# Kernel optimization log

Measured on AMD Instinct MI355X. Metric: run time of the kernel, lower is better.

The kernel has to match this reference:

```python
import jax, jax.numpy as jnp
import numpy as np

B, N, IN_DIM, HID, K = 16, 1024, 512, 256, 3
ALPHA = 0.2  # leaky relu slope
NEG = -9e15  # mask value from original code (-9000000000000000.0)


def setup_inputs() -> dict:
    key = jax.random.key(0)
    ks = jax.random.split(key, 10)
    adj = (jax.random.uniform(ks[0], (B, 3, N, N)) < 0.01).astype(jnp.float32)
    inputs = jax.random.normal(ks[1], (B, N, IN_DIM), dtype=jnp.float32)
    s = 0.07
    W = jax.random.normal(ks[2], (3, K, IN_DIM, HID), dtype=jnp.float32) * s
    # attention vector a [2F,1] split into a1 (for h_i) and a2 (for h_j)
    a1 = jax.random.normal(ks[3], (3, K, HID), dtype=jnp.float32) * s
    a2 = jax.random.normal(ks[4], (3, K, HID), dtype=jnp.float32) * s
    Ww = jax.random.normal(ks[5], (HID, 100), dtype=jnp.float32) * s
    bw = jnp.zeros((100,), dtype=jnp.float32)
    Wc = jax.random.normal(ks[6], (100, 1), dtype=jnp.float32) * s
    return {"adj": adj, "inputs": inputs, "W": W, "a1": a1, "a2": a2,
            "Ww": Ww, "bw": bw, "Wc": Wc}


def _gat(adjp, inputs, W_, a1_, a2_):
    # h = X W : [B,N,F]
    h = jnp.einsum('bni,if->bnf', inputs, W_)
    # e_ij = leakyrelu(a1.h_i + a2.h_j) -- equivalent to the original
    # cat([h_i, h_j]) @ a without materializing the [B,N,N,2F] tensor
    f1 = h @ a1_  # [B,N]
    f2 = h @ a2_  # [B,N]
    e = jax.nn.leaky_relu(f1[:, :, None] + f2[:, None, :], ALPHA)
    att = jax.nn.softmax(jnp.where(adjp > 0, e, NEG), axis=2)
    # (dropout on attention is identity in eval mode)
    return jnp.einsum('bnm,bmf->bnf', att, h)


def reference(adj, inputs, W, a1, a2, Ww, bw, Wc):
    k_layers = W.shape[1]
    # powers[t] holds adj_t^(k+1) for layer k (matmuls(adj, k))
    powers = [adj[:, t] for t in range(3)]
    layer_list = []
    for k in range(k_layers):
        out = 0.0
        for t in range(3):
            out = out + _gat(powers[t], inputs, W[t, k], a1[t, k], a2[t, k])
        layer_list.append(out)
        if k + 1 < k_layers:
            powers = [jnp.matmul(p, adj[:, t]) for t, p in enumerate(powers)]
    H = jnp.stack(layer_list, axis=2)  # [B,N,K,F]
    s = jnp.tanh(H @ Ww + bw) @ Wc     # [B,N,K,1]
    vs = jax.nn.softmax(s[..., 0], axis=2)  # [B,N,K]
    return jnp.einsum('bnk,bnkf->bnf', vs, H)
```

## Files before the change

### kernel.cpp

```cpp
#include <hip/hip_runtime.h>


typedef unsigned long long u64;
typedef __attribute__((ext_vector_type(4))) float f32x4;
typedef __attribute__((ext_vector_type(8))) short bf16x8;

#define NEGF (-9.0e15f)
#define L2E 1.44269504f

__device__ __forceinline__ float fexp2(float x){
#if __has_builtin(__builtin_amdgcn_exp2f)
  return __builtin_amdgcn_exp2f(x);
#else
  return exp2f(x);
#endif
}
__device__ __forceinline__ float frcp(float x){
#if __has_builtin(__builtin_amdgcn_rcpf)
  return __builtin_amdgcn_rcpf(x);
#else
  return 1.0f/x;
#endif
}
__device__ __forceinline__ unsigned short f2bf(float x){
  union { float f; unsigned u; } a; a.f = x;
  unsigned r = a.u + 0x7FFFu + ((a.u >> 16) & 1u);
  return (unsigned short)(r >> 16);
}
__device__ __forceinline__ unsigned pack_bf16x2(float lo, float hi){
  union { float f; unsigned u; } a, b; a.f = lo; b.f = hi;
  unsigned ul = a.u + 0x8000u, uh = b.u + 0x8000u;
#if __has_builtin(__builtin_amdgcn_perm)
  return __builtin_amdgcn_perm(uh, ul, 0x07060302u);
#else
  return (ul >> 16) | (uh & 0xFFFF0000u);
#endif
}
__device__ __forceinline__ float tanh_fast(float x){
  float e = fexp2(x * 2.885390082f);
  return 1.0f - 2.0f*frcp(e + 1.0f);
}
__device__ __forceinline__ void async_cp16(void* lds, const void* g){
  __builtin_amdgcn_global_load_lds(
      (const __attribute__((address_space(1))) unsigned int*)g,
      (__attribute__((address_space(3))) unsigned int*)lds, 16, 0, 0);
}


__global__ void k_build_wb(const float* __restrict__ W, const float* __restrict__ a1,
                           const float* __restrict__ a2, unsigned short* __restrict__ Wb)
{
  int idx = blockIdx.x*256 + threadIdx.x;
  if (idx >= 64*2432) return;
  int c = idx % 2432, g = idx / 2432;
  unsigned short o[8];
  if (c < 2304) {
    int s = c >> 8, f = c & 255, t = s % 3, klq = s / 3;
    const float* wp = W + ((size_t)(t*3 + klq)*512)*256 + f;
#pragma unroll
    for (int e = 0; e < 8; ++e) o[e] = f2bf(wp[(size_t)(g*8 + e)*256]);
  } else if (c < 2322) {
    int c2 = c - 2304, s = c2 >> 1, t = s % 3, klq = s / 3;
    const float* av = ((c2 & 1) ? a2 : a1) + (t*3 + klq)*256;
    const float* wp = W + ((size_t)(t*3 + klq)*512)*256;
#pragma unroll
    for (int e = 0; e < 8; ++e) {
      float acc = 0.0f;
      const float* wr = wp + (size_t)(g*8 + e)*256;
      for (int f = 0; f < 256; ++f) acc += wr[f]*av[f];
      o[e] = f2bf(acc);
    }
  } else {
#pragma unroll
    for (int e = 0; e < 8; ++e) o[e] = 0;
  }
  ushort4 lo, hi;
  lo.x=o[0]; lo.y=o[1]; lo.z=o[2]; lo.w=o[3];
  hi.x=o[4]; hi.y=o[5]; hi.z=o[6]; hi.w=o[7];
  ushort4* dst = (ushort4*)(Wb + (size_t)idx*8);
  dst[0] = lo; dst[1] = hi;
}

__global__ void k_xconv(const float* __restrict__ X, unsigned short* __restrict__ Xs)
{
  int idx = blockIdx.x*256 + threadIdx.x;
  int bn = idx & 16383, g = idx >> 14;
  const float* xp = X + (size_t)bn*512 + g*8;
  ushort4 lo, hi;
  lo.x=f2bf(xp[0]); lo.y=f2bf(xp[1]); lo.z=f2bf(xp[2]); lo.w=f2bf(xp[3]);
  hi.x=f2bf(xp[4]); hi.y=f2bf(xp[5]); hi.z=f2bf(xp[6]); hi.w=f2bf(xp[7]);
  ushort4* dst = (ushort4*)(Xs + (size_t)idx*8);
  dst[0] = lo; dst[1] = hi;
}

__global__ __launch_bounds__(256) void k_bitpack(
    const float* __restrict__ adj, u64* __restrict__ mbA0, u64* __restrict__ mbT)
{
  int gw = blockIdx.x*4 + (threadIdx.x >> 6);
  int lane = threadIdx.x & 63;
#pragma unroll
  for (int r = 0; r < 2; ++r) {
    int row = gw*2 + r;
    int i = row & 1023, bt = row >> 10;
    int t = bt % 3, b = bt / 3;
    int sb = t*16 + b;
    const float* ap = adj + (size_t)row*1024 + lane;
    u64 myw = 0;
#pragma unroll
    for (int w = 0; w < 16; ++w) {
      u64 bal = __ballot(ap[w*64] > 0.0f);
      if (lane == w) myw = bal;
    }
    if (lane < 16) {
      mbA0[((size_t)sb*1024 + i)*16 + lane] = myw;
      mbT[((size_t)sb*16 + lane)*1024 + i] = myw;
    }
  }
}

__global__ void k_boolmm(const u64* __restrict__ A, const u64* __restrict__ Bm,
                         u64* __restrict__ outA, u64* __restrict__ outT, int sbase)
{
  int tid = blockIdx.x*256 + threadIdx.x;
  int w = tid & 15, i = (tid >> 4) & 1023, tb = tid >> 14;
  const u64* Ar = A + ((size_t)tb*1024 + i)*16;
  const u64* Bb = Bm + (size_t)tb*16384;
  u64 acc = 0;
  for (int ww = 0; ww < 16; ++ww) {
    u64 aw = Ar[ww];
    while (aw) {
      int kk = __builtin_ctzll(aw);
      aw &= aw - 1;
      acc |= Bb[((size_t)(ww*64 + kk))*16 + w];
    }
  }
  if (outA) outA[((size_t)tb*1024 + i)*16 + w] = acc;
  int t = tb >> 4, bq = tb & 15;
  outT[(((size_t)(sbase + t)*16 + bq)*16 + w)*1024 + i] = acc;
}


__global__ __launch_bounds__(256) void k_gemm_h(
    const unsigned short* __restrict__ Xs, const unsigned short* __restrict__ Wb,
    unsigned short* __restrict__ hsw, float* __restrict__ fbuf,
    float* __restrict__ G1p, float* __restrict__ G2p)
{
  __shared__ unsigned short Asl[8*132*8 + 8];
  __shared__ unsigned short Bsl[8*132*8 + 8];
  const int tid = threadIdx.x, lane = tid & 63, wid = tid >> 6;
  int vb = blockIdx.x;
  int xc = vb & 7, mrest = vb >> 3;
  int mt = xc + 8*(mrest/19), nt = mrest % 19;
  const int M0 = mt << 7, N0 = nt << 7;
  const int wr = (wid >> 1) << 6, wc = (wid & 1) << 6;
  const int me = lane & 15;
  f32x4 acc[4][4] = {};
  for (int ks64 = 0; ks64 < 8; ++ks64) {
    __syncthreads();
#pragma unroll
    for (int c = 0; c < 4; ++c) {
      int chunk = wid*4 + c, g = chunk >> 1, hh = chunk & 1;
      int ldsoff = (g*132 + hh*64)*8;
      const unsigned short* gpA = Xs + ((size_t)(ks64*8 + g)*16384 + (M0 + hh*64 + lane))*8;
      async_cp16(Asl + ldsoff, gpA);
      const unsigned short* gpB = Wb + ((size_t)(ks64*8 + g)*2432 + (N0 + hh*64 + lane))*8;
      async_cp16(Bsl + ldsoff, gpB);
    }
    __syncthreads();
#pragma unroll
    for (int ks32 = 0; ks32 < 2; ++ks32) {
      const int kg = ks32*4 + (lane >> 4);
      bf16x8 afr[4], bfr[4];
#pragma unroll
      for (int rb = 0; rb < 4; ++rb)
        afr[rb] = *(const bf16x8*)(Asl + (kg*132 + wr + rb*16 + me)*8);
#pragma unroll
      for (int cb = 0; cb < 4; ++cb)
        bfr[cb] = *(const bf16x8*)(Bsl + (kg*132 + wc + cb*16 + me)*8);
#pragma unroll
      for (int rb = 0; rb < 4; ++rb)
#pragma unroll
        for (int cb = 0; cb < 4; ++cb)
          acc[rb][cb] = __builtin_amdgcn_mfma_f32_16x16x32_bf16(afr[rb], bfr[cb], acc[rb][cb], 0, 0, 0);
    }
  }
  const int quad = lane >> 4;
#pragma unroll
  for (int rb = 0; rb < 4; ++rb) {
    int jbase = M0 + wr + rb*16 + quad*4;
    int bidx = jbase >> 10, jn = jbase & 1023;
#pragma unroll
    for (int cb = 0; cb < 4; ++cb) {
      int c = N0 + wc + cb*16 + me;
      f32x4 v = acc[rb][cb];
      if (c < 2304) {
        int s = c >> 8, f = c & 255;
        ushort4 pk;
        pk.x = f2bf(v[0]); pk.y = f2bf(v[1]); pk.z = f2bf(v[2]); pk.w = f2bf(v[3]);
        *(ushort4*)(hsw + (size_t)s*4194304 + (size_t)bidx*262144 + ((jn>>3)*256 + f)*8 + (jn&7)) = pk;
      } else if (c < 2322) {
        int c2 = c - 2304, s = c2 >> 1, wh = c2 & 1;
        f32x4 vL = v * L2E;
        if (wh == 0) {
          *(f32x4*)(fbuf + (size_t)s*16384 + jbase) = vL;
        } else {
          f32x4 g1v, g2v;
#pragma unroll
          for (int k = 0; k < 4; ++k) {
            g1v[k] = fexp2(vL[k]);
            g2v[k] = fexp2(0.2f*vL[k]);
          }
          *(f32x4*)(G1p + (size_t)s*16384 + jbase) = g1v;
          *(f32x4*)(G2p + (size_t)s*16384 + jbase) = g2v;
        }
      }
    }
  }
}


__global__ __launch_bounds__(256) void k_rowl(
    const u64* __restrict__ mbT, const float* __restrict__ fbuf,
    const float* __restrict__ G1p, const float* __restrict__ G2p,
    float* __restrict__ rowR1, float* __restrict__ rowR2,
    float* __restrict__ rowRT, float* __restrict__ rowZr)
{
  int lane = threadIdx.x & 63;
  for (int gw = blockIdx.x*4 + (threadIdx.x >> 6); gw < 147456; gw += 18432) {
    int i = gw & 1023, sb = gw >> 10;
    int b = sb & 15, s = sb >> 4;

    const float* g1q = G1p + (size_t)s*16384 + b*1024 + lane*16;
    const float* g2q = G2p + (size_t)s*16384 + b*1024 + lane*16;
    float4 a0 = *(const float4*)(g1q);
    float4 a1 = *(const float4*)(g1q + 4);
    float4 a2 = *(const float4*)(g1q + 8);
    float4 a3 = *(const float4*)(g1q + 12);
    float4 c0 = *(const float4*)(g2q);
    float4 c1 = *(const float4*)(g2q + 4);
    float4 c2 = *(const float4*)(g2q + 8);
    float4 c3 = *(const float4*)(g2q + 12);
    float g1e[16] = {a0.x,a0.y,a0.z,a0.w, a1.x,a1.y,a1.z,a1.w,
                     a2.x,a2.y,a2.z,a2.w, a3.x,a3.y,a3.z,a3.w};
    float g2e[16] = {c0.x,c0.y,c0.z,c0.w, c1.x,c1.y,c1.z,c1.w,
                     c2.x,c2.y,c2.z,c2.w, c3.x,c3.y,c3.z,c3.w};

    u64 word = mbT[(size_t)sb*16384 + (size_t)(lane >> 2)*1024 + i];
    unsigned fld = (unsigned)(word >> ((lane & 3)*16)) & 0xFFFFu;

    float f1i = fbuf[(size_t)s*16384 + b*1024 + i];
    float RT = fexp2(-f1i);

    float S1 = 0.0f, S2 = 0.0f;
#pragma unroll
    for (int e = 0; e < 16; ++e) {
      unsigned m32 = (unsigned)(((int)(fld << (31 - e))) >> 31);
      float t1 = __uint_as_float(__float_as_uint(g1e[e]) & m32);
      float t2 = __uint_as_float(__float_as_uint(g2e[e]) & m32);
      bool c = (g1e[e] >= RT);
      S1 += c ? t1 : 0.0f;
      S2 += c ? 0.0f : t2;
    }
#pragma unroll
    for (int off = 32; off; off >>= 1) {
      S1 += __shfl_xor(S1, off);
      S2 += __shfl_xor(S2, off);
    }
    if (lane == 0) {
      float EF1 = fexp2(f1i);
      float EF2 = fexp2(0.2f*f1i);
      float l = __builtin_fmaf(EF1, S1, EF2*S2);
      float rinv = frcp(l);
      rowR1[gw] = EF1*rinv;
      rowR2[gw] = EF2*rinv;
      rowRT[gw] = RT;
      rowZr[gw] = (l == 0.0f) ? 0.0009765625f : 0.0f;
    }
  }
}


__global__ __launch_bounds__(256, 3) void k_attgemm(
    const unsigned short* __restrict__ hsw,
    const float* __restrict__ G1p, const float* __restrict__ G2p,
    const float* __restrict__ rowR1, const float* __restrict__ rowR2,
    const float* __restrict__ rowRT, const float* __restrict__ rowZr,
    const u64* __restrict__ mbT, float* __restrict__ H32)
{
  __shared__ unsigned short Bts[2*8192];
  const int tid = threadIdx.x, lane = tid & 63, wid = tid >> 6;
  const int me = lane & 15, quad = lane >> 4;
  int vb = blockIdx.x;
  int mt = vb / 48, g = vb % 48;
  int kl = g >> 4, b = g & 15;
  const int i0w = mt*64 + wid*16;
  const int ir0 = i0w + me;
  const unsigned short* hbase = hsw + (size_t)(kl*3)*4194304 + (size_t)b*262144;
  const float* g1b = G1p + (size_t)(kl*3)*16384 + b*1024;
  const float* g2b = G2p + (size_t)(kl*3)*16384 + b*1024;
  const float* R1b = rowR1 + ((kl*3)*16 + b)*1024;
  const float* R2b = rowR2 + ((kl*3)*16 + b)*1024;
  const float* RTb = rowRT + ((kl*3)*16 + b)*1024;
  const float* Zrb = rowZr + ((kl*3)*16 + b)*1024;
  const u64* mb = mbT + (size_t)((kl*3)*16 + b)*16384;

  float R1v, R2v, RTv;
  unsigned Zru;
  f32x4 acc[16] = {};

  {
    const unsigned short* hstage = hbase + wid*2048;
    unsigned short* lb = Bts + wid*2048;
#pragma unroll
    for (int c = 0; c < 4; ++c)
      async_cp16(lb + c*512, hstage + c*512 + lane*8);
  }
  u64 mw = mb[ir0];
  u64 nm = 0;

  for (int it = 0; it < 96; ++it) {
    const int tt = it >> 5, kk = it & 1;
    const int st = (it >> 1) & 15;
    if ((it & 31) == 0) {
      R1v = R1b[tt*16384 + ir0];
      R2v = R2b[tt*16384 + ir0];
      RTv = RTb[tt*16384 + ir0];
      Zru = __float_as_uint(Zrb[tt*16384 + ir0]);
    }
    if (!kk && it) mw = nm;

    __syncthreads();

    if (it + 1 < 96) {
      int nx = it + 1;
      int nt2 = nx >> 5, ns = (nx >> 1) & 15, nk = nx & 1;
      const unsigned short* hstage = hbase + (size_t)nt2*4194304 + ns*16384 + (nk*4 + wid)*2048;
      unsigned short* lb = Bts + nk*8192 + wid*2048;
#pragma unroll
      for (int c = 0; c < 4; ++c)
        async_cp16(lb + c*512, hstage + c*512 + lane*8);
    }
    if (kk && it + 1 < 96) {
      int gid = (it + 1) >> 1;
      int nt2 = gid >> 4, ns = gid & 15;
      nm = mb[(size_t)nt2*262144 + ns*1024 + ir0];
    }

    const int joff = tt*16384 + st*64 + kk*32 + quad*8;
    float4 ga = *(const float4*)(g1b + joff);
    float4 gb4 = *(const float4*)(g1b + joff + 4);
    float4 ha = *(const float4*)(g2b + joff);
    float4 hb4 = *(const float4*)(g2b + joff + 4);
    float g1e[8] = {ga.x, ga.y, ga.z, ga.w, gb4.x, gb4.y, gb4.z, gb4.w};
    float g2e[8] = {ha.x, ha.y, ha.z, ha.w, hb4.x, hb4.y, hb4.z, hb4.w};

    const int kloc = kk*32 + quad*8;
    unsigned mby = (unsigned)((mw >> kloc) & 0xFFull);
    union { bf16x8 v; unsigned u[4]; } ua;
#pragma unroll
    for (int p = 0; p < 4; ++p) {
      float p0, p1;
      {
        const int e = 2*p;
        bool c = (g1e[e] >= RTv);
        float pu = (c ? g1e[e] : g2e[e]) * (c ? R1v : R2v);
        unsigned m32 = (unsigned)(((int)(mby << (31 - e))) >> 31);
        p0 = __uint_as_float((__float_as_uint(pu) & m32) | Zru);
      }
      {
        const int e = 2*p + 1;
        bool c = (g1e[e] >= RTv);
        float pu = (c ? g1e[e] : g2e[e]) * (c ? R1v : R2v);
        unsigned m32 = (unsigned)(((int)(mby << (31 - e))) >> 31);
        p1 = __uint_as_float((__float_as_uint(pu) & m32) | Zru);
      }
      ua.u[p] = pack_bf16x2(p0, p1);
    }
    const unsigned short* bbase = Bts + kk*8192 + quad*2048;
#pragma unroll
    for (int cb = 0; cb < 16; ++cb) {
      bf16x8 bf = *(const bf16x8*)(bbase + (cb*16 + me)*8);
      acc[cb] = __builtin_amdgcn_mfma_f32_16x16x32_bf16(ua.v, bf, acc[cb], 0, 0, 0);
    }
  }

  {
    int io = i0w + quad*4;
#pragma unroll
    for (int cb = 0; cb < 16; ++cb) {
      int f = cb*16 + me;
      float* hp = H32 + (((size_t)b*1024 + io)*3 + kl)*256 + f;
#pragma unroll
      for (int r = 0; r < 4; ++r)
        hp[(size_t)r*768] = acc[cb][r];
    }
  }
}


__global__ __launch_bounds__(256) void k_score(
    const float* __restrict__ H32, const float* __restrict__ Ww,
    const float* __restrict__ bwv, const float* __restrict__ Wcv, float* __restrict__ svals)
{
  __shared__ unsigned short Bs[8*7*64*8];
  __shared__ float bwL[128], WcL[128];
  const int tid = threadIdx.x, lane = tid & 63, wid = tid >> 6;
  const int me = lane & 15, quad = lane >> 4;
  for (int idx = tid; idx < 3584; idx += 256) {
    int kk = idx / 448, rem = idx % 448;
    int cb = rem >> 6, l = rem & 63;
    int n = cb*16 + (l & 15);
    int kbase = kk*32 + (l >> 4)*8;
    ushort4 lo, hi;
    if (n < 100) {
      const float* wp = Ww + (size_t)kbase*100 + n;
      lo.x = f2bf(wp[0]);   lo.y = f2bf(wp[100]); lo.z = f2bf(wp[200]); lo.w = f2bf(wp[300]);
      hi.x = f2bf(wp[400]); hi.y = f2bf(wp[500]); hi.z = f2bf(wp[600]); hi.w = f2bf(wp[700]);
    } else {
      lo.x=lo.y=lo.z=lo.w=0; hi.x=hi.y=hi.z=hi.w=0;
    }
    ushort4* dst = (ushort4*)(Bs + (size_t)idx*8);
    dst[0] = lo; dst[1] = hi;
  }
  if (tid < 128) {
    bwL[tid] = (tid < 100) ? bwv[tid] : 0.0f;
    WcL[tid] = (tid < 100) ? Wcv[tid] : 0.0f;
  }
  __syncthreads();

  const int row0 = blockIdx.x*64 + wid*16;
  const float* Arow = H32 + (size_t)(row0 + me)*256;
  f32x4 acc[7] = {};
#pragma unroll
  for (int kk = 0; kk < 8; ++kk) {
    const float* ap = Arow + kk*32 + quad*8;
    float4 a0 = *(const float4*)(ap);
    float4 a1 = *(const float4*)(ap + 4);
    union { bf16x8 v; unsigned u[4]; } ua;
    ua.u[0] = pack_bf16x2(a0.x, a0.y);
    ua.u[1] = pack_bf16x2(a0.z, a0.w);
    ua.u[2] = pack_bf16x2(a1.x, a1.y);
    ua.u[3] = pack_bf16x2(a1.z, a1.w);
#pragma unroll
    for (int cb = 0; cb < 7; ++cb) {
      bf16x8 bf = *(const bf16x8*)(Bs + ((size_t)(kk*7 + cb)*64 + lane)*8);
      acc[cb] = __builtin_amdgcn_mfma_f32_16x16x32_bf16(ua.v, bf, acc[cb], 0, 0, 0);
    }
  }
#pragma unroll
  for (int r = 0; r < 4; ++r) {
    float contrib = 0.0f;
#pragma unroll
    for (int cb = 0; cb < 7; ++cb) {
      int col = cb*16 + me;
      contrib += tanh_fast(acc[cb][r] + bwL[col]) * WcL[col];
    }
    contrib += __shfl_xor(contrib, 1);
    contrib += __shfl_xor(contrib, 2);
    contrib += __shfl_xor(contrib, 4);
    contrib += __shfl_xor(contrib, 8);
    if (me == 0) svals[row0 + quad*4 + r] = contrib;
  }
}

__global__ void k_combine(const float* __restrict__ svals, const float* __restrict__ H32,
                          float* __restrict__ out)
{
  int tid = blockIdx.x*256 + threadIdx.x;
  int fq = tid & 63, bn = tid >> 6;
  float s0 = svals[bn*3], s1 = svals[bn*3+1], s2 = svals[bn*3+2];
  float mm = fmaxf(s0, fmaxf(s1, s2));
  float e0 = fexp2((s0-mm)*L2E), e1 = fexp2((s1-mm)*L2E), e2 = fexp2((s2-mm)*L2E);
  float inv = frcp(e0 + e1 + e2);
  const f32x4* h0 = (const f32x4*)(H32 + (size_t)bn*768) + fq;
  const f32x4* h1 = (const f32x4*)(H32 + (size_t)bn*768 + 256) + fq;
  const f32x4* h2 = (const f32x4*)(H32 + (size_t)bn*768 + 512) + fq;
  f32x4 r = (e0*(*h0) + e1*(*h1) + e2*(*h2))*inv;
  *((f32x4*)out + (size_t)bn*64 + fq) = r;
}


extern "C" void kernel_launch(void* const* d_in, const int* in_sizes, int n_in,
                              void* d_out, int out_size, void* d_ws, size_t ws_size,
                              hipStream_t stream) {
  const float* adj = (const float*)d_in[0];
  const float* X   = (const float*)d_in[1];
  const float* W   = (const float*)d_in[2];
  const float* a1  = (const float*)d_in[3];
  const float* a2  = (const float*)d_in[4];
  const float* Ww  = (const float*)d_in[5];
  const float* bw  = (const float*)d_in[6];
  const float* Wc  = (const float*)d_in[7];
  float* out = (float*)d_out;
  char* ws = (char*)d_ws;

  unsigned short* Xs  = (unsigned short*)(ws + 0);
  unsigned short* Wb  = (unsigned short*)(ws + 16777216);
  float* H32          = (float*)(ws + 0);
  unsigned short* hsw = (unsigned short*)(ws + 50331648);
  u64* mbA            = (u64*)(ws + 125829120);
  float* rowR1        = (float*)(ws + 125829120);
  float* rowR2        = (float*)(ws + 126418944);
  float* rowRT        = (float*)(ws + 127008768);
  float* rowZr        = (float*)(ws + 127598592);
  u64* mbT            = (u64*)(ws + 138412032);
  float* fbuf         = (float*)(ws + 157286400);
  float* G1p          = (float*)(ws + 158466048);
  float* G2p          = (float*)(ws + 159055872);
  float* svals        = (float*)(ws + 159645696);

  k_build_wb<<<608, 256, 0, stream>>>(W, a1, a2, Wb);
  k_xconv<<<4096, 256, 0, stream>>>(X, Xs);
  k_bitpack<<<6144, 256, 0, stream>>>(adj, mbA, mbT);
  k_boolmm<<<3072, 256, 0, stream>>>(mbA, mbA, mbA + 786432, mbT, 3);
  k_boolmm<<<3072, 256, 0, stream>>>(mbA, mbA + 786432, (u64*)nullptr, mbT, 6);
  k_gemm_h<<<2432, 256, 0, stream>>>(Xs, Wb, hsw, fbuf, G1p, G2p);
  k_rowl<<<4608, 256, 0, stream>>>(mbT, fbuf, G1p, G2p, rowR1, rowR2, rowRT, rowZr);
  k_attgemm<<<768, 256, 0, stream>>>(hsw, G1p, G2p, rowR1, rowR2, rowRT, rowZr, mbT, H32);
  k_score<<<768, 256, 0, stream>>>(H32, Ww, bw, Wc, svals);
  k_combine<<<4096, 256, 0, stream>>>(svals, H32, out);
}
```

Before: 435.0 us.

## Merge prep kernels, overlap first boolean matmul with H GEMM, fuse score+combine

Three independent preprocessing kernels (weight pack, X conversion, adjacency bitpack) are merged into one launch with block-range dispatch. The first boolean adjacency-power kernel now runs as extra blocks of the H GEMM launch so the two can overlap. The score and combine kernels are fused, with 384-thread blocks covering 32 nodes and the scores kept in shared memory. This removes launch gaps and the svals round trip, at the cost of shared-memory allocation in the boolmm blocks and uneven block workloads.

```diff
diff --git a/kernel.cpp b/kernel.cpp
--- a/kernel.cpp
+++ b/kernel.cpp
@@ -47,76 +47,76 @@
 }
 
 
-__global__ void k_build_wb(const float* __restrict__ W, const float* __restrict__ a1,
-                           const float* __restrict__ a2, unsigned short* __restrict__ Wb)
-{
-  int idx = blockIdx.x*256 + threadIdx.x;
-  if (idx >= 64*2432) return;
-  int c = idx % 2432, g = idx / 2432;
-  unsigned short o[8];
-  if (c < 2304) {
-    int s = c >> 8, f = c & 255, t = s % 3, klq = s / 3;
-    const float* wp = W + ((size_t)(t*3 + klq)*512)*256 + f;
-#pragma unroll
-    for (int e = 0; e < 8; ++e) o[e] = f2bf(wp[(size_t)(g*8 + e)*256]);
-  } else if (c < 2322) {
-    int c2 = c - 2304, s = c2 >> 1, t = s % 3, klq = s / 3;
-    const float* av = ((c2 & 1) ? a2 : a1) + (t*3 + klq)*256;
-    const float* wp = W + ((size_t)(t*3 + klq)*512)*256;
-#pragma unroll
-    for (int e = 0; e < 8; ++e) {
-      float acc = 0.0f;
-      const float* wr = wp + (size_t)(g*8 + e)*256;
-      for (int f = 0; f < 256; ++f) acc += wr[f]*av[f];
-      o[e] = f2bf(acc);
-    }
-  } else {
-#pragma unroll
-    for (int e = 0; e < 8; ++e) o[e] = 0;
-  }
-  ushort4 lo, hi;
-  lo.x=o[0]; lo.y=o[1]; lo.z=o[2]; lo.w=o[3];
-  hi.x=o[4]; hi.y=o[5]; hi.z=o[6]; hi.w=o[7];
-  ushort4* dst = (ushort4*)(Wb + (size_t)idx*8);
-  dst[0] = lo; dst[1] = hi;
-}
-
-__global__ void k_xconv(const float* __restrict__ X, unsigned short* __restrict__ Xs)
-{
-  int idx = blockIdx.x*256 + threadIdx.x;
-  int bn = idx & 16383, g = idx >> 14;
-  const float* xp = X + (size_t)bn*512 + g*8;
-  ushort4 lo, hi;
-  lo.x=f2bf(xp[0]); lo.y=f2bf(xp[1]); lo.z=f2bf(xp[2]); lo.w=f2bf(xp[3]);
-  hi.x=f2bf(xp[4]); hi.y=f2bf(xp[5]); hi.z=f2bf(xp[6]); hi.w=f2bf(xp[7]);
-  ushort4* dst = (ushort4*)(Xs + (size_t)idx*8);
-  dst[0] = lo; dst[1] = hi;
-}
-
-__global__ __launch_bounds__(256) void k_bitpack(
+__global__ __launch_bounds__(256) void k_prep(
+    const float* __restrict__ W, const float* __restrict__ a1,
+    const float* __restrict__ a2, unsigned short* __restrict__ Wb,
+    const float* __restrict__ X, unsigned short* __restrict__ Xs,
     const float* __restrict__ adj, u64* __restrict__ mbA0, u64* __restrict__ mbT)
 {
-  int gw = blockIdx.x*4 + (threadIdx.x >> 6);
-  int lane = threadIdx.x & 63;
-#pragma unroll
-  for (int r = 0; r < 2; ++r) {
-    int row = gw*2 + r;
-    int i = row & 1023, bt = row >> 10;
-    int t = bt % 3, b = bt / 3;
-    int sb = t*16 + b;
-    const float* ap = adj + (size_t)row*1024 + lane;
-    u64 myw = 0;
-#pragma unroll
-    for (int w = 0; w < 16; ++w) {
-      u64 bal = __ballot(ap[w*64] > 0.0f);
-      if (lane == w) myw = bal;
-    }
-    if (lane < 16) {
-      mbA0[((size_t)sb*1024 + i)*16 + lane] = myw;
-      mbT[((size_t)sb*16 + lane)*1024 + i] = myw;
-    }
-  }
-}
+  if (blockIdx.x < 608) {
+    int idx = blockIdx.x*256 + threadIdx.x;
+    if (idx >= 64*2432) return;
+    int c = idx % 2432, g = idx / 2432;
+    unsigned short o[8];
+    if (c < 2304) {
+      int s = c >> 8, f = c & 255, t = s % 3, klq = s / 3;
+      const float* wp = W + ((size_t)(t*3 + klq)*512)*256 + f;
+#pragma unroll
+      for (int e = 0; e < 8; ++e) o[e] = f2bf(wp[(size_t)(g*8 + e)*256]);
+    } else if (c < 2322) {
+      int c2 = c - 2304, s = c2 >> 1, t = s % 3, klq = s / 3;
+      const float* av = ((c2 & 1) ? a2 : a1) + (t*3 + klq)*256;
+      const float* wp = W + ((size_t)(t*3 + klq)*512)*256;
+#pragma unroll
+      for (int e = 0; e < 8; ++e) {
+        float acc = 0.0f;
+        const float* wr = wp + (size_t)(g*8 + e)*256;
+        for (int f = 0; f < 256; ++f) acc += wr[f]*av[f];
+        o[e] = f2bf(acc);
+      }
+    } else {
+#pragma unroll
+      for (int e = 0; e < 8; ++e) o[e] = 0;
+    }
+    ushort4 lo, hi;
+    lo.x=o[0]; lo.y=o[1]; lo.z=o[2]; lo.w=o[3];
+    hi.x=o[4]; hi.y=o[5]; hi.z=o[6]; hi.w=o[7];
+    ushort4* dst = (ushort4*)(Wb + (size_t)idx*8);
+    dst[0] = lo; dst[1] = hi;
+  } else if (blockIdx.x < 4704) {
+    int idx = (blockIdx.x - 608)*256 + threadIdx.x;
+    int bn = idx & 16383, g = idx >> 14;
+    const float* xp = X + (size_t)bn*512 + g*8;
+    ushort4 lo, hi;
+    lo.x=f2bf(xp[0]); lo.y=f2bf(xp[1]); lo.z=f2bf(xp[2]); lo.w=f2bf(xp[3]);
+    hi.x=f2bf(xp[4]); hi.y=f2bf(xp[5]); hi.z=f2bf(xp[6]); hi.w=f2bf(xp[7]);
+    ushort4* dst = (ushort4*)(Xs + (size_t)idx*8);
+    dst[0] = lo; dst[1] = hi;
+  } else {
+    int vb = blockIdx.x - 4704;
+    int gw = vb*4 + (threadIdx.x >> 6);
+    int lane = threadIdx.x & 63;
+#pragma unroll
+    for (int r = 0; r < 2; ++r) {
+      int row = gw*2 + r;
+      int i = row & 1023, bt = row >> 10;
+      int t = bt % 3, b = bt / 3;
+      int sb = t*16 + b;
+      const float* ap = adj + (size_t)row*1024 + lane;
+      u64 myw = 0;
+#pragma unroll
+      for (int w = 0; w < 16; ++w) {
+        u64 bal = __ballot(ap[w*64] > 0.0f);
+        if (lane == w) myw = bal;
+      }
+      if (lane < 16) {
+        mbA0[((size_t)sb*1024 + i)*16 + lane] = myw;
+        mbT[((size_t)sb*16 + lane)*1024 + i] = myw;
+      }
+    }
+  }
+}
+
 
 __global__ void k_boolmm(const u64* __restrict__ A, const u64* __restrict__ Bm,
                          u64* __restrict__ outA, u64* __restrict__ outT, int sbase)
@@ -140,13 +140,33 @@
 }
 
 
-__global__ __launch_bounds__(256) void k_gemm_h(
+__global__ __launch_bounds__(256) void k_mid(
     const unsigned short* __restrict__ Xs, const unsigned short* __restrict__ Wb,
     unsigned short* __restrict__ hsw, float* __restrict__ fbuf,
-    float* __restrict__ G1p, float* __restrict__ G2p)
+    float* __restrict__ G1p, float* __restrict__ G2p,
+    const u64* __restrict__ mbA0, u64* __restrict__ outA1, u64* __restrict__ mbT)
 {
   __shared__ unsigned short Asl[8*132*8 + 8];
   __shared__ unsigned short Bsl[8*132*8 + 8];
+  if (blockIdx.x >= 2432) {
+    int tid = (blockIdx.x - 2432)*256 + threadIdx.x;
+    int w = tid & 15, i = (tid >> 4) & 1023, tb = tid >> 14;
+    const u64* Ar = mbA0 + ((size_t)tb*1024 + i)*16;
+    const u64* Bb = mbA0 + (size_t)tb*16384;
+    u64 acc = 0;
+    for (int ww = 0; ww < 16; ++ww) {
+      u64 aw = Ar[ww];
+      while (aw) {
+        int kk = __builtin_ctzll(aw);
+        aw &= aw - 1;
+        acc |= Bb[((size_t)(ww*64 + kk))*16 + w];
+      }
+    }
+    outA1[((size_t)tb*1024 + i)*16 + w] = acc;
+    int t = tb >> 4, bq = tb & 15;
+    mbT[(((size_t)(3 + t)*16 + bq)*16 + w)*1024 + i] = acc;
+    return;
+  }
   const int tid = threadIdx.x, lane = tid & 63, wid = tid >> 6;
   int vb = blockIdx.x;
   int xc = vb & 7, mrest = vb >> 3;
@@ -398,15 +418,17 @@
 }
 
 
-__global__ __launch_bounds__(256) void k_score(
+__global__ __launch_bounds__(384) void k_scorecomb(
     const float* __restrict__ H32, const float* __restrict__ Ww,
-    const float* __restrict__ bwv, const float* __restrict__ Wcv, float* __restrict__ svals)
+    const float* __restrict__ bwv, const float* __restrict__ Wcv,
+    float* __restrict__ out)
 {
   __shared__ unsigned short Bs[8*7*64*8];
   __shared__ float bwL[128], WcL[128];
+  __shared__ float svL[96];
   const int tid = threadIdx.x, lane = tid & 63, wid = tid >> 6;
   const int me = lane & 15, quad = lane >> 4;
-  for (int idx = tid; idx < 3584; idx += 256) {
+  for (int idx = tid; idx < 3584; idx += 384) {
     int kk = idx / 448, rem = idx % 448;
     int cb = rem >> 6, l = rem & 63;
     int n = cb*16 + (l & 15);
@@ -428,7 +450,7 @@
   }
   __syncthreads();
 
-  const int row0 = blockIdx.x*64 + wid*16;
+  const int row0 = blockIdx.x*96 + wid*16;
   const float* Arow = H32 + (size_t)(row0 + me)*256;
   f32x4 acc[7] = {};
 #pragma unroll
@@ -459,24 +481,24 @@
     contrib += __shfl_xor(contrib, 2);
     contrib += __shfl_xor(contrib, 4);
     contrib += __shfl_xor(contrib, 8);
-    if (me == 0) svals[row0 + quad*4 + r] = contrib;
-  }
-}
-
-__global__ void k_combine(const float* __restrict__ svals, const float* __restrict__ H32,
-                          float* __restrict__ out)
-{
-  int tid = blockIdx.x*256 + threadIdx.x;
-  int fq = tid & 63, bn = tid >> 6;
-  float s0 = svals[bn*3], s1 = svals[bn*3+1], s2 = svals[bn*3+2];
-  float mm = fmaxf(s0, fmaxf(s1, s2));
-  float e0 = fexp2((s0-mm)*L2E), e1 = fexp2((s1-mm)*L2E), e2 = fexp2((s2-mm)*L2E);
-  float inv = frcp(e0 + e1 + e2);
-  const f32x4* h0 = (const f32x4*)(H32 + (size_t)bn*768) + fq;
-  const f32x4* h1 = (const f32x4*)(H32 + (size_t)bn*768 + 256) + fq;
-  const f32x4* h2 = (const f32x4*)(H32 + (size_t)bn*768 + 512) + fq;
-  f32x4 r = (e0*(*h0) + e1*(*h1) + e2*(*h2))*inv;
-  *((f32x4*)out + (size_t)bn*64 + fq) = r;
+    if (me == 0) svL[wid*16 + quad*4 + r] = contrib;
+  }
+  __syncthreads();
+
+  const int bn0 = blockIdx.x*32;
+  for (int idx = tid; idx < 2048; idx += 384) {
+    int fq = idx & 63, bl = idx >> 6;
+    int bn = bn0 + bl;
+    float s0 = svL[bl*3], s1 = svL[bl*3+1], s2 = svL[bl*3+2];
+    float mm = fmaxf(s0, fmaxf(s1, s2));
+    float e0 = fexp2((s0-mm)*L2E), e1 = fexp2((s1-mm)*L2E), e2 = fexp2((s2-mm)*L2E);
+    float inv = frcp(e0 + e1 + e2);
+    const f32x4* h0 = (const f32x4*)(H32 + (size_t)bn*768) + fq;
+    const f32x4* h1 = (const f32x4*)(H32 + (size_t)bn*768 + 256) + fq;
+    const f32x4* h2 = (const f32x4*)(H32 + (size_t)bn*768 + 512) + fq;
+    f32x4 r = (e0*(*h0) + e1*(*h1) + e2*(*h2))*inv;
+    *((f32x4*)out + (size_t)bn*64 + fq) = r;
+  }
 }
 
 
@@ -507,16 +529,11 @@
   float* fbuf         = (float*)(ws + 157286400);
   float* G1p          = (float*)(ws + 158466048);
   float* G2p          = (float*)(ws + 159055872);
-  float* svals        = (float*)(ws + 159645696);
-
-  k_build_wb<<<608, 256, 0, stream>>>(W, a1, a2, Wb);
-  k_xconv<<<4096, 256, 0, stream>>>(X, Xs);
-  k_bitpack<<<6144, 256, 0, stream>>>(adj, mbA, mbT);
-  k_boolmm<<<3072, 256, 0, stream>>>(mbA, mbA, mbA + 786432, mbT, 3);
+
+  k_prep<<<10848, 256, 0, stream>>>(W, a1, a2, Wb, X, Xs, adj, mbA, mbT);
+  k_mid<<<5504, 256, 0, stream>>>(Xs, Wb, hsw, fbuf, G1p, G2p, mbA, mbA + 786432, mbT);
   k_boolmm<<<3072, 256, 0, stream>>>(mbA, mbA + 786432, (u64*)nullptr, mbT, 6);
-  k_gemm_h<<<2432, 256, 0, stream>>>(Xs, Wb, hsw, fbuf, G1p, G2p);
   k_rowl<<<4608, 256, 0, stream>>>(mbT, fbuf, G1p, G2p, rowR1, rowR2, rowRT, rowZr);
   k_attgemm<<<768, 256, 0, stream>>>(hsw, G1p, G2p, rowR1, rowR2, rowRT, rowZr, mbT, H32);
-  k_score<<<768, 256, 0, stream>>>(H32, Ww, bw, Wc, svals);
-  k_combine<<<4096, 256, 0, stream>>>(svals, H32, out);
-}
+  k_scorecomb<<<512, 384, 0, stream>>>(H32, Ww, bw, Wc, out);
+}
```

After: 448.5 us. 1.03x slower.
